# Kernel tuning notes

Hardware: AMD Instinct MI355X
Metric: run time of the kernel (lower is better)

## Reference

```python
import jax, jax.numpy as jnp
import numpy as np

N_NODES = 50000


def sage_conv(x, src, dst, Wl, bl, Wr):
    # mean-aggregate neighbor features: message from src -> dst
    msg = x[src]                                            # [E, d]
    agg = jax.ops.segment_sum(msg, dst, num_segments=N_NODES)
    deg = jax.ops.segment_sum(jnp.ones((src.shape[0],), x.dtype), dst,
                              num_segments=N_NODES)
    mean = agg / jnp.clip(deg, 1.0)[:, None]                # [N, d]
    # PyG SAGEConv: lin_l(mean) + lin_r(x); lin_l has bias, lin_r does not
    return mean @ Wl.T + bl + x @ Wr.T


def setup_inputs() -> dict:
    key = jax.random.key(0)
    ks = jax.random.split(key, 10)
    d_in, d_h = 128, 256
    E = 800000
    x = jax.random.normal(ks[0], (N_NODES, d_in), jnp.float32)
    edge_index = jax.random.randint(ks[1], (2, E), 0, N_NODES, jnp.int32)
    s = 0.05
    return {
        "x": x,
        "edge_index": edge_index,
        "W1_l": jax.random.normal(ks[2], (d_h, d_in), jnp.float32) * s,
        "b1": jax.random.normal(ks[3], (d_h,), jnp.float32) * s,
        "W1_r": jax.random.normal(ks[4], (d_h, d_in), jnp.float32) * s,
        "W2_l": jax.random.normal(ks[5], (d_h, d_h), jnp.float32) * s,
        "b2": jax.random.normal(ks[6], (d_h,), jnp.float32) * s,
        "W2_r": jax.random.normal(ks[7], (d_h, d_h), jnp.float32) * s,
        "head_w": jax.random.normal(ks[8], (1, d_h), jnp.float32) * s,
        "head_b": jax.random.normal(ks[9], (1,), jnp.float32) * s,
    }


def reference(x, edge_index, W1_l, b1, W1_r, W2_l, b2, W2_r, head_w, head_b):
    src, dst = edge_index[0], edge_index[1]
    h = jax.nn.relu(sage_conv(x, src, dst, W1_l, b1, W1_r))
    # dropout is identity in eval mode
    h = jax.nn.relu(sage_conv(h, src, dst, W2_l, b2, W2_r))
    out = h @ head_w.T + head_b                              # [N, 1]
    return out[:, 0]                                         # [N]
```

## Files before the change

### kernel.cpp

```cpp
#include <hip/hip_runtime.h>
#include <hip/hip_bf16.h>
#include <hip/hip_fp8.h>

#define D_IN 128
#define D_H  256
#define NBLK 128
#define BSH  7
#define BNODES 128
#define MAXCH 6400

typedef __attribute__((ext_vector_type(8))) short short8;
typedef __attribute__((ext_vector_type(4))) float floatx4;

__device__ __forceinline__ unsigned short f2bf(float f) {
    __hip_bfloat16 h = __float2bfloat16(f);
    return *reinterpret_cast<unsigned short*>(&h);
}
__device__ __forceinline__ float bf2f(unsigned short s) {
    union { unsigned int u; float f; } v;
    v.u = ((unsigned int)s) << 16;
    return v.f;
}
__device__ __forceinline__ unsigned char f2fp8(float f) {
    __hip_fp8_e4m3 t(f);
    return (unsigned char)t.__x;
}

__device__ __forceinline__ void excl_scan512(int* vals, int NB, int* part) {
    const int t = threadIdx.x;
    const int i0 = t * 2, i1 = t * 2 + 1;
    int v0 = (i0 < NB) ? vals[i0] : 0;
    int v1 = (i1 < NB) ? vals[i1] : 0;
    part[t] = v0 + v1;
    __syncthreads();
    for (int off = 1; off < 256; off <<= 1) {
        int u = (t >= off) ? part[t - off] : 0;
        __syncthreads();
        part[t] += u;
        __syncthreads();
    }
    const int pre = (t == 0) ? 0 : part[t - 1];
    if (i0 < NB) vals[i0] = pre;
    if (i1 < NB) vals[i1] = pre + v0;
    __syncthreads();
}

__global__ void p1_hist_conv_k(const int* __restrict__ dst, int* __restrict__ cnt2d,
                               int E, int NB,
                               const float* __restrict__ x, unsigned short* __restrict__ xb,
                               unsigned char* __restrict__ xb8, int nx4,
                               const float* __restrict__ w1l, unsigned short* __restrict__ w1lb,
                               const float* __restrict__ w1r, unsigned short* __restrict__ w1rb, int nw14,
                               const float* __restrict__ w2l, unsigned short* __restrict__ w2lb,
                               const float* __restrict__ w2r, unsigned short* __restrict__ w2rb, int nw24) {
    if (blockIdx.x < NBLK) {
        __shared__ int h[512];
        for (int i = threadIdx.x; i < NB; i += 256) h[i] = 0;
        __syncthreads();
        const int CH = (E + NBLK - 1) / NBLK;
        const int e0 = blockIdx.x * CH;
        const int e1 = min(e0 + CH, E);
        for (int e = e0 + threadIdx.x; e < e1; e += 256)
            atomicAdd(&h[dst[e] >> BSH], 1);
        __syncthreads();
        for (int i = threadIdx.x; i < NB; i += 256)
            cnt2d[blockIdx.x * NB + i] = h[i];
        return;
    }
    int i = (blockIdx.x - NBLK) * 256 + threadIdx.x;
    if (i < nx4) {
        float4 v = ((const float4*)x)[i];
        ushort4 u;
        u.x = f2bf(v.x); u.y = f2bf(v.y); u.z = f2bf(v.z); u.w = f2bf(v.w);
        ((ushort4*)xb)[i] = u;
        uchar4 c;
        c.x = f2fp8(v.x); c.y = f2fp8(v.y); c.z = f2fp8(v.z); c.w = f2fp8(v.w);
        ((uchar4*)xb8)[i] = c;
        return;
    }
    i -= nx4;
    const float* s; unsigned short* d; int k;
    if (i < nw14) { s = w1l; d = w1lb; k = i; }
    else {
        i -= nw14;
        if (i < nw14) { s = w1r; d = w1rb; k = i; }
        else {
            i -= nw14;
            if (i < nw24) { s = w2l; d = w2lb; k = i; }
            else {
                i -= nw24;
                if (i >= nw24) return;
                s = w2r; d = w2rb; k = i;
            }
        }
    }
    float4 v = ((const float4*)s)[k];
    ushort4 u;
    u.x = f2bf(v.x); u.y = f2bf(v.y); u.z = f2bf(v.z); u.w = f2bf(v.w);
    ((ushort4*)d)[k] = u;
}

__global__ __launch_bounds__(NBLK) void bucket_scan_k(const int* __restrict__ cnt2d,
                                                      int* __restrict__ off2d,
                                                      int* __restrict__ tot, int NB) {
    const int B = blockIdx.x, t = threadIdx.x;
    __shared__ int sc[NBLK];
    __shared__ int orig[NBLK];
    int v = cnt2d[t * NB + B];
    orig[t] = v; sc[t] = v;
    __syncthreads();
    for (int off = 1; off < NBLK; off <<= 1) {
        int u = (t >= off) ? sc[t - off] : 0;
        __syncthreads();
        sc[t] += u;
        __syncthreads();
    }
    off2d[t * NB + B] = sc[t] - orig[t];
    if (t == NBLK - 1) tot[B] = sc[t];
}

__global__ __launch_bounds__(256) void place_k(const int* __restrict__ src,
                                               const int* __restrict__ dst,
                                               const int* __restrict__ off2d,
                                               const int* __restrict__ tot,
                                               unsigned int* __restrict__ staging,
                                               int E, int NB) {
    __shared__ unsigned int lstage[MAXCH];
    __shared__ int lstart[512], lcur[512], runstart[512];
    __shared__ int part[256];
    const int b = blockIdx.x, tid = threadIdx.x;
    const int CH = (E + NBLK - 1) / NBLK;
    const int e0 = b * CH;
    const int e1 = min(e0 + CH, E);
    const int n = e1 - e0;

    for (int i = tid; i < NB; i += 256) { lstart[i] = 0; runstart[i] = tot[i]; }
    __syncthreads();
    for (int e = e0 + tid; e < e1; e += 256)
        atomicAdd(&lstart[dst[e] >> BSH], 1);
    __syncthreads();
    excl_scan512(lstart, NB, part);
    excl_scan512(runstart, NB, part);
    for (int i = tid; i < NB; i += 256) {
        runstart[i] += off2d[b * NB + i];
        lcur[i] = lstart[i];
    }
    __syncthreads();
    for (int e = e0 + tid; e < e1; e += 256) {
        const int d = dst[e];
        const int pos = atomicAdd(&lcur[d >> BSH], 1);
        lstage[pos] = ((unsigned int)d << 16) | (unsigned int)src[e];
    }
    __syncthreads();
    for (int i = tid; i < n; i += 256) {
        const unsigned int u = lstage[i];
        const int bkt = (int)(u >> (16 + BSH));
        staging[runstart[bkt] + (i - lstart[bkt])] = u;
    }
}

__global__ __launch_bounds__(256) void bucket_sort_k(const unsigned int* __restrict__ staging,
                                                     const int* __restrict__ tot,
                                                     int* __restrict__ rp, int* __restrict__ col,
                                                     int M, int NB) {
    const int B = blockIdx.x, tid = threadIdx.x;
    __shared__ int red[256];
    __shared__ int h[BNODES], sc[BNODES], cur[BNODES];
    __shared__ int s0s, s1s;
    int acc = 0;
    for (int i = tid; i < B; i += 256) acc += tot[i];
    red[tid] = acc; __syncthreads();
    for (int off = 128; off > 0; off >>= 1) {
        if (tid < off) red[tid] += red[tid + off];
        __syncthreads();
    }
    if (tid == 0) { s0s = red[0]; s1s = red[0] + tot[B]; }
    if (tid < BNODES) h[tid] = 0;
    __syncthreads();
    const int s0 = s0s, s1 = s1s;
    for (int i = s0 + tid; i < s1; i += 256)
        atomicAdd(&h[(staging[i] >> 16) & (BNODES - 1)], 1);
    __syncthreads();
    if (tid < BNODES) sc[tid] = h[tid];
    __syncthreads();
    for (int off = 1; off < BNODES; off <<= 1) {
        int v = 0;
        if (tid < BNODES && tid >= off) v = sc[tid - off];
        __syncthreads();
        if (tid < BNODES) sc[tid] += v;
        __syncthreads();
    }
    if (tid < BNODES) {
        const int excl = sc[tid] - h[tid];
        const int node = B * BNODES + tid;
        if (node < M) rp[node] = s0 + excl;
        cur[tid] = s0 + excl;
    }
    if (B == NB - 1 && tid == 0) rp[M] = s1;
    __syncthreads();
    for (int i = s0 + tid; i < s1; i += 256) {
        const unsigned int u = staging[i];
        const int pos = atomicAdd(&cur[(u >> 16) & (BNODES - 1)], 1);
        col[pos] = (int)(u & 0xFFFFu);
    }
}

template <int UNP>
__device__ __forceinline__ int agg1_stage(const unsigned char* __restrict__ X8,
                                          const int* __restrict__ col,
                                          int j, int e, int sel, int l32, float* acc) {
    for (; j + 2 * UNP <= e; j += 2 * UNP) {
        int c0[UNP], c1[UNP];
#pragma unroll
        for (int u = 0; u < UNP; ++u) { c0[u] = col[j + 2 * u]; c1[u] = col[j + 2 * u + 1]; }
        unsigned int vals[UNP];
#pragma unroll
        for (int u = 0; u < UNP; ++u) {
            const int cs = sel ? c1[u] : c0[u];
            vals[u] = *(const unsigned int*)(X8 + (size_t)cs * 128 + l32 * 4);
        }
#pragma unroll
        for (int u = 0; u < UNP; ++u) {
            __hip_fp8x4_e4m3 p;
            p.__x = vals[u];
            float4 f = (float4)p;
            acc[0] += f.x; acc[1] += f.y; acc[2] += f.z; acc[3] += f.w;
        }
    }
    return j;
}

__global__ __launch_bounds__(256) void aggregate1_k(
    const unsigned char* __restrict__ X8, const int* __restrict__ col,
    const int* __restrict__ rp, unsigned short* __restrict__ out, int Mnodes) {
    int node = __builtin_amdgcn_readfirstlane((blockIdx.x << 2) + (threadIdx.x >> 6));
    if (node >= Mnodes) return;
    const int lane = threadIdx.x & 63;
    const int sel = lane >> 5;
    const int l32 = lane & 31;
    const int s = rp[node], e = rp[node + 1];
    float acc[4] = {0.f, 0.f, 0.f, 0.f};

    int j = s;
    j = agg1_stage<4>(X8, col, j, e, sel, l32, acc);
    j = agg1_stage<2>(X8, col, j, e, sel, l32, acc);
    j = agg1_stage<1>(X8, col, j, e, sel, l32, acc);
    if (j < e) {
        const int c0 = col[j];
        if (sel == 0) {
            unsigned int v = *(const unsigned int*)(X8 + (size_t)c0 * 128 + l32 * 4);
            __hip_fp8x4_e4m3 p;
            p.__x = v;
            float4 f = (float4)p;
            acc[0] += f.x; acc[1] += f.y; acc[2] += f.z; acc[3] += f.w;
        }
    }
#pragma unroll
    for (int k = 0; k < 4; ++k) acc[k] += __shfl_xor(acc[k], 32, 64);
    const float inv = 1.f / fmaxf((float)(e - s), 1.f);
    if (sel == 0) {
        ushort4 o;
        o.x = f2bf(acc[0] * inv); o.y = f2bf(acc[1] * inv);
        o.z = f2bf(acc[2] * inv); o.w = f2bf(acc[3] * inv);
        *(ushort4*)(out + (size_t)node * 128 + l32 * 4) = o;
    }
}

template <int UN>
__device__ __forceinline__ int agg_stage_fp8(const unsigned char* __restrict__ X8,
                                             const int* __restrict__ col,
                                             int j, int e, int lane, float* acc) {
    for (; j + UN <= e; j += UN) {
        int cs[UN];
#pragma unroll
        for (int u = 0; u < UN; ++u) cs[u] = col[j + u];
        unsigned int vals[UN];
#pragma unroll
        for (int u = 0; u < UN; ++u)
            vals[u] = *(const unsigned int*)(X8 + (size_t)cs[u] * 256 + lane * 4);
#pragma unroll
        for (int u = 0; u < UN; ++u) {
            __hip_fp8x4_e4m3 p;
            p.__x = vals[u];
            float4 f = (float4)p;
            acc[0] += f.x; acc[1] += f.y; acc[2] += f.z; acc[3] += f.w;
        }
    }
    return j;
}

__global__ __launch_bounds__(256) void aggregate2_k(
    const unsigned char* __restrict__ X8, const int* __restrict__ col,
    const int* __restrict__ rp, unsigned short* __restrict__ out, int Mnodes) {
    int node = __builtin_amdgcn_readfirstlane((blockIdx.x << 2) + (threadIdx.x >> 6));
    if (node >= Mnodes) return;
    const int lane = threadIdx.x & 63;
    const int s = rp[node], e = rp[node + 1];
    float acc[4] = {0.f, 0.f, 0.f, 0.f};

    int j = s;
    j = agg_stage_fp8<8>(X8, col, j, e, lane, acc);
    j = agg_stage_fp8<4>(X8, col, j, e, lane, acc);
    j = agg_stage_fp8<2>(X8, col, j, e, lane, acc);
    j = agg_stage_fp8<1>(X8, col, j, e, lane, acc);

    const float inv = 1.f / fmaxf((float)(e - s), 1.f);
    ushort4 o;
    o.x = f2bf(acc[0] * inv); o.y = f2bf(acc[1] * inv);
    o.z = f2bf(acc[2] * inv); o.w = f2bf(acc[3] * inv);
    *(ushort4*)(out + (size_t)node * 256 + lane * 4) = o;
}

template <int K, bool HEAD>
__global__ __launch_bounds__(256, 2) void gemm_mfma_k(
    const unsigned short* __restrict__ A1, const unsigned short* __restrict__ W1,
    const unsigned short* __restrict__ A2, const unsigned short* __restrict__ W2,
    const float* __restrict__ bias, unsigned short* __restrict__ Hout,
    unsigned char* __restrict__ Hout8,
    const float* __restrict__ hw, const float* __restrict__ hb,
    float* __restrict__ out, int M) {
    __shared__ __align__(16) unsigned short sA[128 * 40];
    __shared__ __align__(16) unsigned short sB[256 * 40];
    __shared__ float head_acc[128];

    constexpr int NCK = K / 32;
    constexpr int NC = 2 * NCK;

    const int tid = threadIdx.x;
    const int wave = tid >> 6;
    const int lane = tid & 63;
    const int c = lane & 15;
    const int q = lane >> 4;
    const int m0 = blockIdx.x * 128;

    if (HEAD && tid < 128) head_acc[tid] = 0.f;

    floatx4 acc[8][4];
#pragma unroll
    for (int mi = 0; mi < 8; ++mi)
#pragma unroll
        for (int ni = 0; ni < 4; ++ni) acc[mi][ni] = (floatx4){0.f, 0.f, 0.f, 0.f};

    const int arow = tid >> 1;
    const int aseg = (tid & 1) * 16;
    const int brow = tid >> 2;
    const int bseg = (tid & 3) * 8;
    int gr = m0 + arow;
    if (gr >= M) gr = M - 1;

    auto loadChunk = [&](int t, short8& a0, short8& a1, short8* b) {
        const unsigned short* Ap = (t >= NCK) ? A2 : A1;
        const unsigned short* Wp = (t >= NCK) ? W2 : W1;
        const int k0 = (t & (NCK - 1)) * 32;
        a0 = *(const short8*)(Ap + (size_t)gr * K + k0 + aseg);
        a1 = *(const short8*)(Ap + (size_t)gr * K + k0 + aseg + 8);
#pragma unroll
        for (int i = 0; i < 4; ++i)
            b[i] = *(const short8*)(Wp + (size_t)(brow + i * 64) * K + k0 + bseg);
    };

    short8 ca0, ca1, cb[4], na0, na1, nb[4];
    loadChunk(0, ca0, ca1, cb);

#pragma unroll 1
    for (int t = 0; t < NC; ++t) {
        __syncthreads();
        *(short8*)&sA[arow * 40 + aseg] = ca0;
        *(short8*)&sA[arow * 40 + aseg + 8] = ca1;
#pragma unroll
        for (int i = 0; i < 4; ++i)
            *(short8*)&sB[(brow + i * 64) * 40 + bseg] = cb[i];
        if (t + 1 < NC)
            loadChunk(t + 1, na0, na1, nb);
        __syncthreads();

        short8 af[8], bf[4];
#pragma unroll
        for (int mi = 0; mi < 8; ++mi)
            af[mi] = *(const short8*)&sA[(mi * 16 + c) * 40 + q * 8];
#pragma unroll
        for (int ni = 0; ni < 4; ++ni)
            bf[ni] = *(const short8*)&sB[(wave * 64 + ni * 16 + c) * 40 + q * 8];
#pragma unroll
        for (int mi = 0; mi < 8; ++mi)
#pragma unroll
            for (int ni = 0; ni < 4; ++ni)
                acc[mi][ni] = __builtin_amdgcn_mfma_f32_16x16x32_bf16(
                    af[mi], bf[ni], acc[mi][ni], 0, 0, 0);

        ca0 = na0; ca1 = na1;
#pragma unroll
        for (int i = 0; i < 4; ++i) cb[i] = nb[i];
    }

    if (!HEAD) {
#pragma unroll
        for (int mi = 0; mi < 8; ++mi)
#pragma unroll
            for (int ni = 0; ni < 4; ++ni) {
                const int n = wave * 64 + ni * 16 + c;
                const float bv = bias[n];
#pragma unroll
                for (int reg = 0; reg < 4; ++reg) {
                    const int m = m0 + mi * 16 + q * 4 + reg;
                    if (m < M) {
                        float v = fmaxf(acc[mi][ni][reg] + bv, 0.f);
                        Hout[(size_t)m * 256 + n] = f2bf(v);
                        Hout8[(size_t)m * 256 + n] = f2fp8(v);
                    }
                }
            }
    } else {
#pragma unroll
        for (int mi = 0; mi < 8; ++mi) {
            float p[4] = {0.f, 0.f, 0.f, 0.f};
#pragma unroll
            for (int ni = 0; ni < 4; ++ni) {
                const int n = wave * 64 + ni * 16 + c;
                const float bv = bias[n];
                const float hv = hw[n];
#pragma unroll
                for (int reg = 0; reg < 4; ++reg)
                    p[reg] += fmaxf(acc[mi][ni][reg] + bv, 0.f) * hv;
            }
#pragma unroll
            for (int reg = 0; reg < 4; ++reg) {
                float v = p[reg];
                v += __shfl_xor(v, 1, 64);
                v += __shfl_xor(v, 2, 64);
                v += __shfl_xor(v, 4, 64);
                v += __shfl_xor(v, 8, 64);
                if (c == 0) atomicAdd(&head_acc[mi * 16 + q * 4 + reg], v);
            }
        }
        __syncthreads();
        if (tid < 128) {
            const int m = m0 + tid;
            if (m < M) out[m] = head_acc[tid] + hb[0];
        }
    }
}

extern "C" void kernel_launch(void* const* d_in, const int* in_sizes, int n_in,
                              void* d_out, int out_size, void* d_ws, size_t ws_size,
                              hipStream_t stream) {
    const float* x    = (const float*)d_in[0];
    const int*   ei   = (const int*)d_in[1];
    const float* W1l  = (const float*)d_in[2];
    const float* b1   = (const float*)d_in[3];
    const float* W1r  = (const float*)d_in[4];
    const float* W2l  = (const float*)d_in[5];
    const float* b2   = (const float*)d_in[6];
    const float* W2r  = (const float*)d_in[7];
    const float* hw   = (const float*)d_in[8];
    const float* hb   = (const float*)d_in[9];
    float* out = (float*)d_out;

    const int M = in_sizes[0] / D_IN;
    const int E = in_sizes[1] / 2;
    const int* src = ei;
    const int* dst = ei + E;
    const int NB = (M + BNODES - 1) / BNODES;

    size_t off = 0;
    auto alloc = [&](size_t bytes) -> void* {
        void* p = (char*)d_ws + off;
        off += (bytes + 255) & ~(size_t)255;
        return p;
    };
    int* cnt2d = (int*)alloc((size_t)NBLK * NB * 4);
    int* off2d = (int*)alloc((size_t)NBLK * NB * 4);
    int* tot   = (int*)alloc((size_t)NB * 4);
    unsigned int* staging = (unsigned int*)alloc((size_t)E * 4);
    int* rp    = (int*)alloc((size_t)(M + 1) * 4);
    int* col   = (int*)alloc((size_t)E * 4);
    unsigned short* xb    = (unsigned short*)alloc((size_t)M * D_IN * 2);
    unsigned char*  xb8   = (unsigned char*)alloc((size_t)M * D_IN);
    unsigned short* w1lb  = (unsigned short*)alloc((size_t)D_H * D_IN * 2);
    unsigned short* w1rb  = (unsigned short*)alloc((size_t)D_H * D_IN * 2);
    unsigned short* w2lb  = (unsigned short*)alloc((size_t)D_H * D_H * 2);
    unsigned short* w2rb  = (unsigned short*)alloc((size_t)D_H * D_H * 2);
    unsigned short* mean1 = (unsigned short*)alloc((size_t)M * D_IN * 2);
    unsigned short* h1    = (unsigned short*)alloc((size_t)M * D_H * 2);
    unsigned char*  h8    = (unsigned char*)alloc((size_t)M * D_H);
    unsigned short* mean2 = (unsigned short*)alloc((size_t)M * D_H * 2);

    const int nx4 = (M * D_IN) / 4;
    const int nw14 = (D_H * D_IN) / 4;
    const int nw24 = (D_H * D_H) / 4;
    const int tot4 = nx4 + 2 * nw14 + 2 * nw24;
    const int convblk = (tot4 + 255) / 256;
    p1_hist_conv_k<<<NBLK + convblk, 256, 0, stream>>>(
        dst, cnt2d, E, NB,
        x, xb, xb8, nx4, W1l, w1lb, W1r, w1rb, nw14, W2l, w2lb, W2r, w2rb, nw24);
    bucket_scan_k<<<NB, NBLK, 0, stream>>>(cnt2d, off2d, tot, NB);
    place_k<<<NBLK, 256, 0, stream>>>(src, dst, off2d, tot, staging, E, NB);
    bucket_sort_k<<<NB, 256, 0, stream>>>(staging, tot, rp, col, M, NB);

    const int nblk = (M + 127) / 128;
    const int ablk = (M + 3) / 4;

    aggregate1_k<<<ablk, 256, 0, stream>>>(xb8, col, rp, mean1, M);
    gemm_mfma_k<D_IN, false><<<nblk, 256, 0, stream>>>(
        mean1, w1lb, xb, w1rb, b1, h1, h8, nullptr, nullptr, nullptr, M);

    aggregate2_k<<<ablk, 256, 0, stream>>>(h8, col, rp, mean2, M);
    gemm_mfma_k<D_H, true><<<nblk, 256, 0, stream>>>(
        mean2, w2lb, h1, w2rb, b2, nullptr, nullptr, hw, hb, out, M);
}
```

Baseline: 233.4 us.

## Store fp8 features in 64-column chunks and aggregate per chunk via grid y

The fp8 copies of x and h1 are now written in a chunk-major layout (64-byte column slices per node), and one templated aggregation kernel processes each chunk as a separate grid-y slice. Each wave handles four neighbors at a time with 16 lanes each, so every gather is a 64-byte row segment. The goal is a smaller per-chunk working set for the random gathers, which should improve L2/MALL cache hit rates. The cost is re-reading the CSR column indices once per chunk and extra shuffle reductions. Separately, place_k reuses the per-block histogram from cnt2d instead of recounting destinations with LDS atomics.

```diff
diff --git a/kernel.cpp b/kernel.cpp
--- a/kernel.cpp
+++ b/kernel.cpp
@@ -15,11 +15,6 @@
 __device__ __forceinline__ unsigned short f2bf(float f) {
     __hip_bfloat16 h = __float2bfloat16(f);
     return *reinterpret_cast<unsigned short*>(&h);
-}
-__device__ __forceinline__ float bf2f(unsigned short s) {
-    union { unsigned int u; float f; } v;
-    v.u = ((unsigned int)s) << 16;
-    return v.f;
 }
 __device__ __forceinline__ unsigned char f2fp8(float f) {
     __hip_fp8_e4m3 t(f);
@@ -75,7 +70,11 @@
         ((ushort4*)xb)[i] = u;
         uchar4 c;
         c.x = f2fp8(v.x); c.y = f2fp8(v.y); c.z = f2fp8(v.z); c.w = f2fp8(v.w);
-        ((uchar4*)xb8)[i] = c;
+        const int Mn = nx4 >> 5;
+        const int node = i >> 5;
+        const int w = i & 31;
+        const int chunk = w >> 4;
+        *(uchar4*)(xb8 + ((size_t)chunk * Mn + node) * 64 + (w & 15) * 4) = c;
         return;
     }
     i -= nx4;
@@ -121,6 +120,7 @@
 
 __global__ __launch_bounds__(256) void place_k(const int* __restrict__ src,
                                                const int* __restrict__ dst,
+                                               const int* __restrict__ cnt2d,
                                                const int* __restrict__ off2d,
                                                const int* __restrict__ tot,
                                                unsigned int* __restrict__ staging,
@@ -134,10 +134,10 @@
     const int e1 = min(e0 + CH, E);
     const int n = e1 - e0;
 
-    for (int i = tid; i < NB; i += 256) { lstart[i] = 0; runstart[i] = tot[i]; }
-    __syncthreads();
-    for (int e = e0 + tid; e < e1; e += 256)
-        atomicAdd(&lstart[dst[e] >> BSH], 1);
+    for (int i = tid; i < NB; i += 256) {
+        lstart[i] = cnt2d[b * NB + i];
+        runstart[i] = tot[i];
+    }
     __syncthreads();
     excl_scan512(lstart, NB, part);
     excl_scan512(runstart, NB, part);
@@ -205,110 +205,57 @@
     }
 }
 
-template <int UNP>
-__device__ __forceinline__ int agg1_stage(const unsigned char* __restrict__ X8,
-                                          const int* __restrict__ col,
-                                          int j, int e, int sel, int l32, float* acc) {
-    for (; j + 2 * UNP <= e; j += 2 * UNP) {
-        int c0[UNP], c1[UNP];
-#pragma unroll
-        for (int u = 0; u < UNP; ++u) { c0[u] = col[j + 2 * u]; c1[u] = col[j + 2 * u + 1]; }
-        unsigned int vals[UNP];
-#pragma unroll
-        for (int u = 0; u < UNP; ++u) {
-            const int cs = sel ? c1[u] : c0[u];
-            vals[u] = *(const unsigned int*)(X8 + (size_t)cs * 128 + l32 * 4);
-        }
-#pragma unroll
-        for (int u = 0; u < UNP; ++u) {
-            __hip_fp8x4_e4m3 p;
-            p.__x = vals[u];
-            float4 f = (float4)p;
-            acc[0] += f.x; acc[1] += f.y; acc[2] += f.z; acc[3] += f.w;
-        }
-    }
-    return j;
-}
-
-__global__ __launch_bounds__(256) void aggregate1_k(
+template <int K>
+__global__ __launch_bounds__(256) void aggregate_chunked_k(
     const unsigned char* __restrict__ X8, const int* __restrict__ col,
     const int* __restrict__ rp, unsigned short* __restrict__ out, int Mnodes) {
-    int node = __builtin_amdgcn_readfirstlane((blockIdx.x << 2) + (threadIdx.x >> 6));
+    const int node = __builtin_amdgcn_readfirstlane((blockIdx.x << 2) + (threadIdx.x >> 6));
     if (node >= Mnodes) return;
+    const int chunk = blockIdx.y;
+    const unsigned char* base = X8 + (size_t)chunk * Mnodes * 64;
     const int lane = threadIdx.x & 63;
-    const int sel = lane >> 5;
-    const int l32 = lane & 31;
+    const int g = lane >> 4;
+    const int q = lane & 15;
     const int s = rp[node], e = rp[node + 1];
-    float acc[4] = {0.f, 0.f, 0.f, 0.f};
+    float a0 = 0.f, a1 = 0.f, a2 = 0.f, a3 = 0.f;
 
     int j = s;
-    j = agg1_stage<4>(X8, col, j, e, sel, l32, acc);
-    j = agg1_stage<2>(X8, col, j, e, sel, l32, acc);
-    j = agg1_stage<1>(X8, col, j, e, sel, l32, acc);
+    for (; j + 8 <= e; j += 8) {
+        const int c0 = col[j + g];
+        const int c1 = col[j + 4 + g];
+        const unsigned int v0 = *(const unsigned int*)(base + (size_t)c0 * 64 + q * 4);
+        const unsigned int v1 = *(const unsigned int*)(base + (size_t)c1 * 64 + q * 4);
+        __hip_fp8x4_e4m3 p0; p0.__x = v0; float4 f0 = (float4)p0;
+        __hip_fp8x4_e4m3 p1; p1.__x = v1; float4 f1 = (float4)p1;
+        a0 += f0.x; a1 += f0.y; a2 += f0.z; a3 += f0.w;
+        a0 += f1.x; a1 += f1.y; a2 += f1.z; a3 += f1.w;
+    }
+    for (; j + 4 <= e; j += 4) {
+        const int c0 = col[j + g];
+        const unsigned int v0 = *(const unsigned int*)(base + (size_t)c0 * 64 + q * 4);
+        __hip_fp8x4_e4m3 p0; p0.__x = v0; float4 f0 = (float4)p0;
+        a0 += f0.x; a1 += f0.y; a2 += f0.z; a3 += f0.w;
+    }
     if (j < e) {
-        const int c0 = col[j];
-        if (sel == 0) {
-            unsigned int v = *(const unsigned int*)(X8 + (size_t)c0 * 128 + l32 * 4);
-            __hip_fp8x4_e4m3 p;
-            p.__x = v;
-            float4 f = (float4)p;
-            acc[0] += f.x; acc[1] += f.y; acc[2] += f.z; acc[3] += f.w;
+        const int jj = j + g;
+        const int cc = col[jj < e ? jj : s];
+        const unsigned int v = *(const unsigned int*)(base + (size_t)cc * 64 + q * 4);
+        if (jj < e) {
+            __hip_fp8x4_e4m3 p; p.__x = v; float4 f = (float4)p;
+            a0 += f.x; a1 += f.y; a2 += f.z; a3 += f.w;
         }
     }
-#pragma unroll
-    for (int k = 0; k < 4; ++k) acc[k] += __shfl_xor(acc[k], 32, 64);
-    const float inv = 1.f / fmaxf((float)(e - s), 1.f);
-    if (sel == 0) {
+    a0 += __shfl_xor(a0, 16, 64); a0 += __shfl_xor(a0, 32, 64);
+    a1 += __shfl_xor(a1, 16, 64); a1 += __shfl_xor(a1, 32, 64);
+    a2 += __shfl_xor(a2, 16, 64); a2 += __shfl_xor(a2, 32, 64);
+    a3 += __shfl_xor(a3, 16, 64); a3 += __shfl_xor(a3, 32, 64);
+    if (g == 0) {
+        const float inv = 1.f / fmaxf((float)(e - s), 1.f);
         ushort4 o;
-        o.x = f2bf(acc[0] * inv); o.y = f2bf(acc[1] * inv);
-        o.z = f2bf(acc[2] * inv); o.w = f2bf(acc[3] * inv);
-        *(ushort4*)(out + (size_t)node * 128 + l32 * 4) = o;
-    }
-}
-
-template <int UN>
-__device__ __forceinline__ int agg_stage_fp8(const unsigned char* __restrict__ X8,
-                                             const int* __restrict__ col,
-                                             int j, int e, int lane, float* acc) {
-    for (; j + UN <= e; j += UN) {
-        int cs[UN];
-#pragma unroll
-        for (int u = 0; u < UN; ++u) cs[u] = col[j + u];
-        unsigned int vals[UN];
-#pragma unroll
-        for (int u = 0; u < UN; ++u)
-            vals[u] = *(const unsigned int*)(X8 + (size_t)cs[u] * 256 + lane * 4);
-#pragma unroll
-        for (int u = 0; u < UN; ++u) {
-            __hip_fp8x4_e4m3 p;
-            p.__x = vals[u];
-            float4 f = (float4)p;
-            acc[0] += f.x; acc[1] += f.y; acc[2] += f.z; acc[3] += f.w;
-        }
-    }
-    return j;
-}
-
-__global__ __launch_bounds__(256) void aggregate2_k(
-    const unsigned char* __restrict__ X8, const int* __restrict__ col,
-    const int* __restrict__ rp, unsigned short* __restrict__ out, int Mnodes) {
-    int node = __builtin_amdgcn_readfirstlane((blockIdx.x << 2) + (threadIdx.x >> 6));
-    if (node >= Mnodes) return;
-    const int lane = threadIdx.x & 63;
-    const int s = rp[node], e = rp[node + 1];
-    float acc[4] = {0.f, 0.f, 0.f, 0.f};
-
-    int j = s;
-    j = agg_stage_fp8<8>(X8, col, j, e, lane, acc);
-    j = agg_stage_fp8<4>(X8, col, j, e, lane, acc);
-    j = agg_stage_fp8<2>(X8, col, j, e, lane, acc);
-    j = agg_stage_fp8<1>(X8, col, j, e, lane, acc);
-
-    const float inv = 1.f / fmaxf((float)(e - s), 1.f);
-    ushort4 o;
-    o.x = f2bf(acc[0] * inv); o.y = f2bf(acc[1] * inv);
-    o.z = f2bf(acc[2] * inv); o.w = f2bf(acc[3] * inv);
-    *(ushort4*)(out + (size_t)node * 256 + lane * 4) = o;
+        o.x = f2bf(a0 * inv); o.y = f2bf(a1 * inv);
+        o.z = f2bf(a2 * inv); o.w = f2bf(a3 * inv);
+        *(ushort4*)(out + (size_t)node * K + chunk * 64 + q * 4) = o;
+    }
 }
 
 template <int K, bool HEAD>
@@ -406,7 +353,7 @@
                     if (m < M) {
                         float v = fmaxf(acc[mi][ni][reg] + bv, 0.f);
                         Hout[(size_t)m * 256 + n] = f2bf(v);
-                        Hout8[(size_t)m * 256 + n] = f2fp8(v);
+                        Hout8[((size_t)wave * M + m) * 64 + (ni * 16 + c)] = f2fp8(v);
                     }
                 }
             }
@@ -494,17 +441,17 @@
         dst, cnt2d, E, NB,
         x, xb, xb8, nx4, W1l, w1lb, W1r, w1rb, nw14, W2l, w2lb, W2r, w2rb, nw24);
     bucket_scan_k<<<NB, NBLK, 0, stream>>>(cnt2d, off2d, tot, NB);
-    place_k<<<NBLK, 256, 0, stream>>>(src, dst, off2d, tot, staging, E, NB);
+    place_k<<<NBLK, 256, 0, stream>>>(src, dst, cnt2d, off2d, tot, staging, E, NB);
     bucket_sort_k<<<NB, 256, 0, stream>>>(staging, tot, rp, col, M, NB);
 
     const int nblk = (M + 127) / 128;
     const int ablk = (M + 3) / 4;
 
-    aggregate1_k<<<ablk, 256, 0, stream>>>(xb8, col, rp, mean1, M);
+    aggregate_chunked_k<D_IN><<<dim3(ablk, 2), 256, 0, stream>>>(xb8, col, rp, mean1, M);
     gemm_mfma_k<D_IN, false><<<nblk, 256, 0, stream>>>(
         mean1, w1lb, xb, w1rb, b1, h1, h8, nullptr, nullptr, nullptr, M);
 
-    aggregate2_k<<<ablk, 256, 0, stream>>>(h8, col, rp, mean2, M);
+    aggregate_chunked_k<D_H><<<dim3(ablk, 4), 256, 0, stream>>>(h8, col, rp, mean2, M);
     gemm_mfma_k<D_H, true><<<nblk, 256, 0, stream>>>(
         mean2, w2lb, h1, w2rb, b2, nullptr, nullptr, hw, hb, out, M);
 }
```

New measurement: 288.4 us. +23.6%, slower.

## Drop bf16 copy of x, reuse histogram counts, add nontemporal loads/stores

Applied to the files above, without the earlier changes.

Stops writing a bf16 copy of x in the conversion kernel. The first GEMM now reads fp32 x directly and converts it to bf16 inside its load path. place_k reuses the per-block bucket counts already computed in cnt2d instead of re-histogramming dst. Nontemporal loads and stores are added for col indices, the mean outputs and the h1 writes to reduce cache pollution. The trade-off is that the GEMM reads twice the bytes for its x operand and does extra conversion work.

```diff
diff --git a/kernel.cpp b/kernel.cpp
--- a/kernel.cpp
+++ b/kernel.cpp
@@ -11,15 +11,11 @@
 
 typedef __attribute__((ext_vector_type(8))) short short8;
 typedef __attribute__((ext_vector_type(4))) float floatx4;
+typedef __attribute__((ext_vector_type(4))) unsigned short ushortx4;
 
 __device__ __forceinline__ unsigned short f2bf(float f) {
     __hip_bfloat16 h = __float2bfloat16(f);
     return *reinterpret_cast<unsigned short*>(&h);
-}
-__device__ __forceinline__ float bf2f(unsigned short s) {
-    union { unsigned int u; float f; } v;
-    v.u = ((unsigned int)s) << 16;
-    return v.f;
 }
 __device__ __forceinline__ unsigned char f2fp8(float f) {
     __hip_fp8_e4m3 t(f);
@@ -47,7 +43,7 @@
 
 __global__ void p1_hist_conv_k(const int* __restrict__ dst, int* __restrict__ cnt2d,
                                int E, int NB,
-                               const float* __restrict__ x, unsigned short* __restrict__ xb,
+                               const float* __restrict__ x,
                                unsigned char* __restrict__ xb8, int nx4,
                                const float* __restrict__ w1l, unsigned short* __restrict__ w1lb,
                                const float* __restrict__ w1r, unsigned short* __restrict__ w1rb, int nw14,
@@ -70,9 +66,6 @@
     int i = (blockIdx.x - NBLK) * 256 + threadIdx.x;
     if (i < nx4) {
         float4 v = ((const float4*)x)[i];
-        ushort4 u;
-        u.x = f2bf(v.x); u.y = f2bf(v.y); u.z = f2bf(v.z); u.w = f2bf(v.w);
-        ((ushort4*)xb)[i] = u;
         uchar4 c;
         c.x = f2fp8(v.x); c.y = f2fp8(v.y); c.z = f2fp8(v.z); c.w = f2fp8(v.w);
         ((uchar4*)xb8)[i] = c;
@@ -121,6 +114,7 @@
 
 __global__ __launch_bounds__(256) void place_k(const int* __restrict__ src,
                                                const int* __restrict__ dst,
+                                               const int* __restrict__ cnt2d,
                                                const int* __restrict__ off2d,
                                                const int* __restrict__ tot,
                                                unsigned int* __restrict__ staging,
@@ -134,10 +128,10 @@
     const int e1 = min(e0 + CH, E);
     const int n = e1 - e0;
 
-    for (int i = tid; i < NB; i += 256) { lstart[i] = 0; runstart[i] = tot[i]; }
-    __syncthreads();
-    for (int e = e0 + tid; e < e1; e += 256)
-        atomicAdd(&lstart[dst[e] >> BSH], 1);
+    for (int i = tid; i < NB; i += 256) {
+        lstart[i] = cnt2d[b * NB + i];
+        runstart[i] = tot[i];
+    }
     __syncthreads();
     excl_scan512(lstart, NB, part);
     excl_scan512(runstart, NB, part);
@@ -212,7 +206,10 @@
     for (; j + 2 * UNP <= e; j += 2 * UNP) {
         int c0[UNP], c1[UNP];
 #pragma unroll
-        for (int u = 0; u < UNP; ++u) { c0[u] = col[j + 2 * u]; c1[u] = col[j + 2 * u + 1]; }
+        for (int u = 0; u < UNP; ++u) {
+            c0[u] = __builtin_nontemporal_load(col + j + 2 * u);
+            c1[u] = __builtin_nontemporal_load(col + j + 2 * u + 1);
+        }
         unsigned int vals[UNP];
 #pragma unroll
         for (int u = 0; u < UNP; ++u) {
@@ -259,10 +256,10 @@
     for (int k = 0; k < 4; ++k) acc[k] += __shfl_xor(acc[k], 32, 64);
     const float inv = 1.f / fmaxf((float)(e - s), 1.f);
     if (sel == 0) {
-        ushort4 o;
+        ushortx4 o;
         o.x = f2bf(acc[0] * inv); o.y = f2bf(acc[1] * inv);
         o.z = f2bf(acc[2] * inv); o.w = f2bf(acc[3] * inv);
-        *(ushort4*)(out + (size_t)node * 128 + l32 * 4) = o;
+        __builtin_nontemporal_store(o, (ushortx4*)(out + (size_t)node * 128 + l32 * 4));
     }
 }
 
@@ -273,7 +270,7 @@
     for (; j + UN <= e; j += UN) {
         int cs[UN];
 #pragma unroll
-        for (int u = 0; u < UN; ++u) cs[u] = col[j + u];
+        for (int u = 0; u < UN; ++u) cs[u] = __builtin_nontemporal_load(col + j + u);
         unsigned int vals[UN];
 #pragma unroll
         for (int u = 0; u < UN; ++u)
@@ -305,16 +302,17 @@
     j = agg_stage_fp8<1>(X8, col, j, e, lane, acc);
 
     const float inv = 1.f / fmaxf((float)(e - s), 1.f);
-    ushort4 o;
+    ushortx4 o;
     o.x = f2bf(acc[0] * inv); o.y = f2bf(acc[1] * inv);
     o.z = f2bf(acc[2] * inv); o.w = f2bf(acc[3] * inv);
-    *(ushort4*)(out + (size_t)node * 256 + lane * 4) = o;
-}
-
-template <int K, bool HEAD>
+    __builtin_nontemporal_store(o, (ushortx4*)(out + (size_t)node * 256 + lane * 4));
+}
+
+template <int K, bool HEAD, bool A2F32>
 __global__ __launch_bounds__(256, 2) void gemm_mfma_k(
     const unsigned short* __restrict__ A1, const unsigned short* __restrict__ W1,
-    const unsigned short* __restrict__ A2, const unsigned short* __restrict__ W2,
+    const unsigned short* __restrict__ A2, const float* __restrict__ A2f,
+    const unsigned short* __restrict__ W2,
     const float* __restrict__ bias, unsigned short* __restrict__ Hout,
     unsigned char* __restrict__ Hout8,
     const float* __restrict__ hw, const float* __restrict__ hb,
@@ -349,11 +347,23 @@
     if (gr >= M) gr = M - 1;
 
     auto loadChunk = [&](int t, short8& a0, short8& a1, short8* b) {
-        const unsigned short* Ap = (t >= NCK) ? A2 : A1;
         const unsigned short* Wp = (t >= NCK) ? W2 : W1;
         const int k0 = (t & (NCK - 1)) * 32;
-        a0 = *(const short8*)(Ap + (size_t)gr * K + k0 + aseg);
-        a1 = *(const short8*)(Ap + (size_t)gr * K + k0 + aseg + 8);
+        if (A2F32 && t >= NCK) {
+            const float* p = A2f + (size_t)gr * K + k0 + aseg;
+            float4 u0 = *(const float4*)(p);
+            float4 u1 = *(const float4*)(p + 4);
+            float4 u2 = *(const float4*)(p + 8);
+            float4 u3 = *(const float4*)(p + 12);
+            a0 = (short8){(short)f2bf(u0.x), (short)f2bf(u0.y), (short)f2bf(u0.z), (short)f2bf(u0.w),
+                          (short)f2bf(u1.x), (short)f2bf(u1.y), (short)f2bf(u1.z), (short)f2bf(u1.w)};
+            a1 = (short8){(short)f2bf(u2.x), (short)f2bf(u2.y), (short)f2bf(u2.z), (short)f2bf(u2.w),
+                          (short)f2bf(u3.x), (short)f2bf(u3.y), (short)f2bf(u3.z), (short)f2bf(u3.w)};
+        } else {
+            const unsigned short* Ap = (t >= NCK) ? A2 : A1;
+            a0 = *(const short8*)(Ap + (size_t)gr * K + k0 + aseg);
+            a1 = *(const short8*)(Ap + (size_t)gr * K + k0 + aseg + 8);
+        }
 #pragma unroll
         for (int i = 0; i < 4; ++i)
             b[i] = *(const short8*)(Wp + (size_t)(brow + i * 64) * K + k0 + bseg);
@@ -405,7 +415,7 @@
                     const int m = m0 + mi * 16 + q * 4 + reg;
                     if (m < M) {
                         float v = fmaxf(acc[mi][ni][reg] + bv, 0.f);
-                        Hout[(size_t)m * 256 + n] = f2bf(v);
+                        __builtin_nontemporal_store(f2bf(v), &Hout[(size_t)m * 256 + n]);
                         Hout8[(size_t)m * 256 + n] = f2fp8(v);
                     }
                 }
@@ -474,7 +484,6 @@
     unsigned int* staging = (unsigned int*)alloc((size_t)E * 4);
     int* rp    = (int*)alloc((size_t)(M + 1) * 4);
     int* col   = (int*)alloc((size_t)E * 4);
-    unsigned short* xb    = (unsigned short*)alloc((size_t)M * D_IN * 2);
     unsigned char*  xb8   = (unsigned char*)alloc((size_t)M * D_IN);
     unsigned short* w1lb  = (unsigned short*)alloc((size_t)D_H * D_IN * 2);
     unsigned short* w1rb  = (unsigned short*)alloc((size_t)D_H * D_IN * 2);
@@ -492,19 +501,19 @@
     const int convblk = (tot4 + 255) / 256;
     p1_hist_conv_k<<<NBLK + convblk, 256, 0, stream>>>(
         dst, cnt2d, E, NB,
-        x, xb, xb8, nx4, W1l, w1lb, W1r, w1rb, nw14, W2l, w2lb, W2r, w2rb, nw24);
+        x, xb8, nx4, W1l, w1lb, W1r, w1rb, nw14, W2l, w2lb, W2r, w2rb, nw24);
     bucket_scan_k<<<NB, NBLK, 0, stream>>>(cnt2d, off2d, tot, NB);
-    place_k<<<NBLK, 256, 0, stream>>>(src, dst, off2d, tot, staging, E, NB);
+    place_k<<<NBLK, 256, 0, stream>>>(src, dst, cnt2d, off2d, tot, staging, E, NB);
     bucket_sort_k<<<NB, 256, 0, stream>>>(staging, tot, rp, col, M, NB);
 
     const int nblk = (M + 127) / 128;
     const int ablk = (M + 3) / 4;
 
     aggregate1_k<<<ablk, 256, 0, stream>>>(xb8, col, rp, mean1, M);
-    gemm_mfma_k<D_IN, false><<<nblk, 256, 0, stream>>>(
-        mean1, w1lb, xb, w1rb, b1, h1, h8, nullptr, nullptr, nullptr, M);
+    gemm_mfma_k<D_IN, false, true><<<nblk, 256, 0, stream>>>(
+        mean1, w1lb, nullptr, x, w1rb, b1, h1, h8, nullptr, nullptr, nullptr, M);
 
     aggregate2_k<<<ablk, 256, 0, stream>>>(h8, col, rp, mean2, M);
-    gemm_mfma_k<D_H, true><<<nblk, 256, 0, stream>>>(
-        mean2, w2lb, h1, w2rb, b2, nullptr, nullptr, hw, hb, out, M);
-}
+    gemm_mfma_k<D_H, true, false><<<nblk, 256, 0, stream>>>(
+        mean2, w2lb, h1, nullptr, w2rb, b2, nullptr, nullptr, hw, hb, out, M);
+}
```

Result: slower. 241.9 us (+3.6%).
